# Kernel optimization log

Measured on AMD Instinct MI355X. Metric: run time of the kernel, lower is better.

## Reference

```python
import jax, jax.numpy as jnp
import numpy as np
from jax import lax


def fps_indices(points, num_sample):
    """Farthest point sampling. points: [B, C, N] -> indices [B, num_sample] int32.
    Standard PointNet++ algorithm: start at index 0, iteratively pick the point
    farthest (in squared L2) from the already-selected set."""
    B, C, N = points.shape

    def step(carry, _):
        min_d, far = carry  # min_d: [B, N] running min sq-dist, far: [B] current index
        # gather coordinates of current farthest point: [B, C, 1]
        cur = jnp.take_along_axis(points, far[:, None, None].astype(jnp.int32), axis=2)
        d = jnp.sum((points - cur) ** 2, axis=1)  # [B, N]
        min_d = jnp.minimum(min_d, d)
        nxt = jnp.argmax(min_d, axis=1).astype(jnp.int32)  # [B]
        return (min_d, nxt), far

    init = (jnp.full((B, N), 1e10, dtype=points.dtype),
            jnp.zeros((B,), dtype=jnp.int32))
    _, idx = lax.scan(step, init, None, length=num_sample)  # idx: [S, B]
    return idx.T  # [B, S]


def setup_inputs() -> dict:
    key = jax.random.key(0)
    B, C, N = 8, 3, 131072
    points = jax.random.normal(key, (B, C, N), dtype=jnp.float32)
    return {"points": points, "num_sample": 2048}


def reference(points, num_sample):
    B, C, N = points.shape
    idx = fps_indices(points, num_sample)  # [B, S]
    # gather sampled points: [B, C, S]
    gather_idx = jnp.broadcast_to(idx[:, None, :], (B, C, num_sample))
    samples = jnp.take_along_axis(points, gather_idx, axis=2)
    return samples
```

## Files before the change

kernel.cpp:

```cpp
#include <hip/hip_runtime.h>
#include <stdint.h>


#define BATCHES 8
#define NPTS    131072
#define KBLK    64
#define TPB     64
#define CHUNK   (NPTS / KBLK)
#define PPT     (CHUNK / TPB)
#define CAP     64

__global__ __launch_bounds__(TPB) void fps_kernel(
    const float* __restrict__ pts, float* __restrict__ out,
    unsigned long long* __restrict__ ws, int S)
{
    const int gb   = blockIdx.x;
    const int b    = gb & (BATCHES - 1);
    const int blk  = gb >> 3;
    const int lane = threadIdx.x;

    const float* X = pts + (size_t)(b * 3 + 0) * NPTS;
    const float* Y = pts + (size_t)(b * 3 + 1) * NPTS;
    const float* Z = pts + (size_t)(b * 3 + 2) * NPTS;
    float* outb = out + (size_t)b * 3 * S;

    const int base2 = blk * CHUNK + lane * PPT;

    float px[PPT], py[PPT], pz[PPT], md[PPT];
#pragma unroll
    for (int q = 0; q < PPT / 4; ++q) {
        float4 vx = *reinterpret_cast<const float4*>(&X[base2 + 4 * q]);
        float4 vy = *reinterpret_cast<const float4*>(&Y[base2 + 4 * q]);
        float4 vz = *reinterpret_cast<const float4*>(&Z[base2 + 4 * q]);
        px[4*q+0] = vx.x; px[4*q+1] = vx.y; px[4*q+2] = vx.z; px[4*q+3] = vx.w;
        py[4*q+0] = vy.x; py[4*q+1] = vy.y; py[4*q+2] = vy.z; py[4*q+3] = vy.w;
        pz[4*q+0] = vz.x; pz[4*q+1] = vz.y; pz[4*q+2] = vz.z; pz[4*q+3] = vz.w;
    }
#pragma unroll
    for (int k = 0; k < PPT; ++k) md[k] = 1e10f;

    unsigned long long* const agnP[2] = {
        ws + (size_t)b * KBLK,
        ws + (size_t)(BATCHES + b) * KBLK };
    volatile unsigned long long* const fstP[2] = {
        (volatile unsigned long long*)(ws + (size_t)(2 * BATCHES + b) * KBLK),
        (volatile unsigned long long*)(ws + (size_t)(3 * BATCHES + b) * KBLK) };

    float cx = X[0], cy = Y[0], cz = Z[0];
    if (blk == 0 && lane == 0) {
        outb[0]             = cx;
        outb[(size_t)S]     = cy;
        outb[(size_t)2 * S] = cz;
    }

    for (int t = 0; t < S - 1; ++t) {
        float bv = -1.0f;
        int   bk = 0;
#pragma unroll
        for (int k = 0; k < PPT; ++k) {
            float dx = __fsub_rn(px[k], cx);
            float dy = __fsub_rn(py[k], cy);
            float dz = __fsub_rn(pz[k], cz);
            float d  = __fadd_rn(__fadd_rn(__fmul_rn(dx, dx), __fmul_rn(dy, dy)),
                                 __fmul_rn(dz, dz));
            float m  = fminf(md[k], d);
            md[k] = m;
            if (m > bv) { bv = m; bk = k; }
        }
        const int bi = base2 + bk;

        float v = bv;
#pragma unroll
        for (int off = 32; off >= 1; off >>= 1)
            v = fmaxf(v, __shfl_xor(v, off));
        unsigned long long eq = __ballot(bv == v);
        int   flane = __ffsll((unsigned long long)eq) - 1;
        int   widx  = __shfl(bi, flane);

        const unsigned long long tagv = (unsigned long long)(t + 1);
        const unsigned long long mypk =
            ((unsigned long long)__float_as_uint(v) << 32) |
            ((unsigned long long)(unsigned)(0x1FFFF - widx) << 12) | tagv;

        volatile unsigned long long* fst = fstP[t & 1];
        unsigned long long*          agn = agnP[t & 1];

        if (lane == 0) fst[blk] = mypk;

        unsigned long long g;
        {
            int  spins  = 0;
            bool capped = false;
            for (;;) {
                unsigned long long gf = fst[lane];
                bool ok = ((gf & 0xFFFull) == tagv);
                if (capped && !ok) {
                    unsigned long long ga = __hip_atomic_load(&agn[lane],
                        __ATOMIC_RELAXED, __HIP_MEMORY_SCOPE_AGENT);
                    if ((ga & 0xFFFull) == tagv) { gf = ga; ok = true; }
                }
                g = gf;
                if (__all((int)ok)) break;
                if (!capped && ++spins == CAP) {
                    capped = true;
                    if (lane == 0)
                        __hip_atomic_store(&agn[blk], mypk,
                            __ATOMIC_RELAXED, __HIP_MEMORY_SCOPE_AGENT);
                }
            }
        }

        float gv = __uint_as_float((unsigned)(g >> 32));
        float m2 = gv;
#pragma unroll
        for (int off = 32; off >= 1; off >>= 1)
            m2 = fmaxf(m2, __shfl_xor(m2, off));
        unsigned long long eq2 = __ballot(gv == m2);
        int fl = __ffsll((unsigned long long)eq2) - 1;
        unsigned long long win = __shfl(g, fl);

        int far = 0x1FFFF - (int)((win >> 12) & 0x1FFFF);
        far = __builtin_amdgcn_readfirstlane(far);

        cx = X[far]; cy = Y[far]; cz = Z[far];
        if (blk == 0 && lane == 0) {
            outb[(size_t)(t + 1)]         = cx;
            outb[(size_t)S + (t + 1)]     = cy;
            outb[(size_t)2 * S + (t + 1)] = cz;
        }
    }
}

extern "C" void kernel_launch(void* const* d_in, const int* in_sizes, int n_in,
                              void* d_out, int out_size, void* d_ws, size_t ws_size,
                              hipStream_t stream) {
    const float* pts = (const float*)d_in[0];
    float* out = (float*)d_out;
    unsigned long long* ws = (unsigned long long*)d_ws;
    int S = out_size / (BATCHES * 3);

    hipMemsetAsync(d_ws, 0,
                   (size_t)4 * BATCHES * KBLK * sizeof(unsigned long long),
                   stream);

    void* args[] = { (void*)&pts, (void*)&out, (void*)&ws, (void*)&S };
    hipLaunchCooperativeKernel((const void*)fps_kernel,
                               dim3(BATCHES * KBLK), dim3(TPB),
                               args, 0, stream);
}
```

Measured before the change: 3.915 ms.

## Halve grid-wide blocks using two-wave blocks with LDS pre-reduction

After: 7.362 ms. 1.88x slower.

```diff
diff --git a/kernel.cpp b/kernel.cpp
--- a/kernel.cpp
+++ b/kernel.cpp
@@ -3,9 +3,10 @@
 
 
 #define BATCHES 8
+#define KBLK    32
+#define TPB     128
+#define NWAVE   (TPB / 64)
 #define NPTS    131072
-#define KBLK    64
-#define TPB     64
 #define CHUNK   (NPTS / KBLK)
 #define PPT     (CHUNK / TPB)
 #define CAP     64
@@ -17,14 +18,17 @@
     const int gb   = blockIdx.x;
     const int b    = gb & (BATCHES - 1);
     const int blk  = gb >> 3;
-    const int lane = threadIdx.x;
+    const int tid  = threadIdx.x;
+    const int lane = tid & 63;
+    const int wv   = tid >> 6;
+    const int myslot = lane & (KBLK - 1);
 
     const float* X = pts + (size_t)(b * 3 + 0) * NPTS;
     const float* Y = pts + (size_t)(b * 3 + 1) * NPTS;
     const float* Z = pts + (size_t)(b * 3 + 2) * NPTS;
     float* outb = out + (size_t)b * 3 * S;
 
-    const int base2 = blk * CHUNK + lane * PPT;
+    const int base2 = blk * CHUNK + tid * PPT;
 
     float px[PPT], py[PPT], pz[PPT], md[PPT];
 #pragma unroll
@@ -39,6 +43,8 @@
 #pragma unroll
     for (int k = 0; k < PPT; ++k) md[k] = 1e10f;
 
+    __shared__ unsigned long long s_part[2][NWAVE];
+
     unsigned long long* const agnP[2] = {
         ws + (size_t)b * KBLK,
         ws + (size_t)(BATCHES + b) * KBLK };
@@ -47,7 +53,7 @@
         (volatile unsigned long long*)(ws + (size_t)(3 * BATCHES + b) * KBLK) };
 
     float cx = X[0], cy = Y[0], cz = Z[0];
-    if (blk == 0 && lane == 0) {
+    if (blk == 0 && tid == 0) {
         outb[0]             = cx;
         outb[(size_t)S]     = cy;
         outb[(size_t)2 * S] = cz;
@@ -74,36 +80,50 @@
         for (int off = 32; off >= 1; off >>= 1)
             v = fmaxf(v, __shfl_xor(v, off));
         unsigned long long eq = __ballot(bv == v);
-        int   flane = __ffsll((unsigned long long)eq) - 1;
-        int   widx  = __shfl(bi, flane);
+        int flane = __ffsll(eq) - 1;
+        int widx  = __shfl(bi, flane);
+
+        const int par = t & 1;
+        if (lane == 0)
+            s_part[par][wv] =
+                ((unsigned long long)__float_as_uint(v) << 32) |
+                ((unsigned long long)(unsigned)(0x1FFFF - widx) << 12);
+        __syncthreads();
+        unsigned long long bp = s_part[par][0];
+        unsigned long long o1 = s_part[par][1];
+        if (o1 > bp) bp = o1;
 
         const unsigned long long tagv = (unsigned long long)(t + 1);
-        const unsigned long long mypk =
-            ((unsigned long long)__float_as_uint(v) << 32) |
-            ((unsigned long long)(unsigned)(0x1FFFF - widx) << 12) | tagv;
-
-        volatile unsigned long long* fst = fstP[t & 1];
-        unsigned long long*          agn = agnP[t & 1];
-
-        if (lane == 0) fst[blk] = mypk;
+        const unsigned long long mypk = bp | tagv;
+        volatile unsigned long long* fst = fstP[par];
+        unsigned long long*          agn = agnP[par];
+        if (tid == 0) fst[blk] = mypk;
 
         unsigned long long g;
         {
             int  spins  = 0;
             bool capped = false;
+            unsigned long long g0 = fst[myslot];
             for (;;) {
-                unsigned long long gf = fst[lane];
-                bool ok = ((gf & 0xFFFull) == tagv);
-                if (capped && !ok) {
-                    unsigned long long ga = __hip_atomic_load(&agn[lane],
+                unsigned long long g1 = fst[myslot];
+                if (capped && (g0 & 0xFFFull) != tagv) {
+                    unsigned long long ga = __hip_atomic_load(&agn[myslot],
                         __ATOMIC_RELAXED, __HIP_MEMORY_SCOPE_AGENT);
-                    if ((ga & 0xFFFull) == tagv) { gf = ga; ok = true; }
+                    if ((ga & 0xFFFull) == tagv) g0 = ga;
                 }
-                g = gf;
-                if (__all((int)ok)) break;
-                if (!capped && ++spins == CAP) {
+                if (__all((int)((g0 & 0xFFFull) == tagv))) { g = g0; break; }
+                unsigned long long g2 = fst[myslot];
+                if (capped && (g1 & 0xFFFull) != tagv) {
+                    unsigned long long ga = __hip_atomic_load(&agn[myslot],
+                        __ATOMIC_RELAXED, __HIP_MEMORY_SCOPE_AGENT);
+                    if ((ga & 0xFFFull) == tagv) g1 = ga;
+                }
+                if (__all((int)((g1 & 0xFFFull) == tagv))) { g = g1; break; }
+                g0 = g2;
+                spins += 2;
+                if (!capped && spins >= CAP) {
                     capped = true;
-                    if (lane == 0)
+                    if (tid == 0)
                         __hip_atomic_store(&agn[blk], mypk,
                             __ATOMIC_RELAXED, __HIP_MEMORY_SCOPE_AGENT);
                 }
@@ -116,14 +136,14 @@
         for (int off = 32; off >= 1; off >>= 1)
             m2 = fmaxf(m2, __shfl_xor(m2, off));
         unsigned long long eq2 = __ballot(gv == m2);
-        int fl = __ffsll((unsigned long long)eq2) - 1;
+        int fl = __ffsll(eq2) - 1;
         unsigned long long win = __shfl(g, fl);
 
         int far = 0x1FFFF - (int)((win >> 12) & 0x1FFFF);
         far = __builtin_amdgcn_readfirstlane(far);
 
         cx = X[far]; cy = Y[far]; cz = Z[far];
-        if (blk == 0 && lane == 0) {
+        if (blk == 0 && tid == 0) {
             outb[(size_t)(t + 1)]         = cx;
             outb[(size_t)S + (t + 1)]     = cy;
             outb[(size_t)2 * S + (t + 1)] = cz;
```

## Replace all-to-all flag polling with leader reduction and broadcast per batch

Applied to the files above, without the earlier changes.

Result: slower. 5.061 ms (+29.3%).

```diff
diff --git a/kernel.cpp b/kernel.cpp
--- a/kernel.cpp
+++ b/kernel.cpp
@@ -3,12 +3,13 @@
 
 
 #define BATCHES 8
-#define NPTS    131072
 #define KBLK    64
 #define TPB     64
+#define NPTS    131072
 #define CHUNK   (NPTS / KBLK)
 #define PPT     (CHUNK / TPB)
 #define CAP     64
+
 
 __global__ __launch_bounds__(TPB) void fps_kernel(
     const float* __restrict__ pts, float* __restrict__ out,
@@ -39,12 +40,18 @@
 #pragma unroll
     for (int k = 0; k < PPT; ++k) md[k] = 1e10f;
 
-    unsigned long long* const agnP[2] = {
+    unsigned long long* const asl[2] = {
         ws + (size_t)b * KBLK,
-        ws + (size_t)(BATCHES + b) * KBLK };
-    volatile unsigned long long* const fstP[2] = {
-        (volatile unsigned long long*)(ws + (size_t)(2 * BATCHES + b) * KBLK),
-        (volatile unsigned long long*)(ws + (size_t)(3 * BATCHES + b) * KBLK) };
+        ws + 512 + (size_t)b * KBLK };
+    volatile unsigned long long* const fsl[2] = {
+        (volatile unsigned long long*)(ws + 1024 + (size_t)b * KBLK),
+        (volatile unsigned long long*)(ws + 1536 + (size_t)b * KBLK) };
+    volatile unsigned long long* const fbc[2] = {
+        (volatile unsigned long long*)(ws + 2048 + (size_t)b * 8),
+        (volatile unsigned long long*)(ws + 2112 + (size_t)b * 8) };
+    unsigned long long* const abc[2] = {
+        ws + 2176 + (size_t)b * 8,
+        ws + 2240 + (size_t)b * 8 };
 
     float cx = X[0], cy = Y[0], cz = Z[0];
     if (blk == 0 && lane == 0) {
@@ -74,52 +81,79 @@
         for (int off = 32; off >= 1; off >>= 1)
             v = fmaxf(v, __shfl_xor(v, off));
         unsigned long long eq = __ballot(bv == v);
-        int   flane = __ffsll((unsigned long long)eq) - 1;
-        int   widx  = __shfl(bi, flane);
+        int flane = __ffsll(eq) - 1;
+        int widx  = __shfl(bi, flane);
 
+        const int par = t & 1;
         const unsigned long long tagv = (unsigned long long)(t + 1);
         const unsigned long long mypk =
             ((unsigned long long)__float_as_uint(v) << 32) |
             ((unsigned long long)(unsigned)(0x1FFFF - widx) << 12) | tagv;
 
-        volatile unsigned long long* fst = fstP[t & 1];
-        unsigned long long*          agn = agnP[t & 1];
+        if (lane == 0) fsl[par][blk] = mypk;
 
-        if (lane == 0) fst[blk] = mypk;
+        int far;
+        if (blk == 0) {
+            unsigned long long g;
+            {
+                int  spins  = 0;
+                bool capped = false;
+                for (;;) {
+                    unsigned long long gf = fsl[par][lane];
+                    bool ok = ((gf & 0xFFFull) == tagv);
+                    if (capped && !ok) {
+                        unsigned long long ga = __hip_atomic_load(&asl[par][lane],
+                            __ATOMIC_RELAXED, __HIP_MEMORY_SCOPE_AGENT);
+                        if ((ga & 0xFFFull) == tagv) { gf = ga; ok = true; }
+                    }
+                    g = gf;
+                    if (__all((int)ok)) break;
+                    if (!capped && ++spins == CAP) capped = true;
+                }
+            }
+            float gv = __uint_as_float((unsigned)(g >> 32));
+            float m2 = gv;
+#pragma unroll
+            for (int off = 32; off >= 1; off >>= 1)
+                m2 = fmaxf(m2, __shfl_xor(m2, off));
+            unsigned long long eq2 = __ballot(gv == m2);
+            int fl = __ffsll(eq2) - 1;
+            unsigned long long win = __shfl(g, fl);
+            far = 0x1FFFF - (int)((win >> 12) & 0x1FFFF);
 
-        unsigned long long g;
-        {
+            if (lane == 0) {
+                unsigned long long w =
+                    ((unsigned long long)(unsigned)far << 12) | tagv;
+                fbc[par][0] = w;
+                __hip_atomic_store(&abc[par][0], w,
+                                   __ATOMIC_RELAXED, __HIP_MEMORY_SCOPE_AGENT);
+            }
+        } else {
             int  spins  = 0;
             bool capped = false;
             for (;;) {
-                unsigned long long gf = fst[lane];
-                bool ok = ((gf & 0xFFFull) == tagv);
-                if (capped && !ok) {
-                    unsigned long long ga = __hip_atomic_load(&agn[lane],
+                unsigned long long w = fbc[par][0];
+                if ((w & 0xFFFull) == tagv) {
+                    far = (int)((w >> 12) & 0x1FFFF);
+                    break;
+                }
+                if (capped) {
+                    unsigned long long wa = __hip_atomic_load(&abc[par][0],
                         __ATOMIC_RELAXED, __HIP_MEMORY_SCOPE_AGENT);
-                    if ((ga & 0xFFFull) == tagv) { gf = ga; ok = true; }
+                    if ((wa & 0xFFFull) == tagv) {
+                        far = (int)((wa >> 12) & 0x1FFFF);
+                        break;
+                    }
                 }
-                g = gf;
-                if (__all((int)ok)) break;
                 if (!capped && ++spins == CAP) {
                     capped = true;
                     if (lane == 0)
-                        __hip_atomic_store(&agn[blk], mypk,
+                        __hip_atomic_store(&asl[par][blk], mypk,
                             __ATOMIC_RELAXED, __HIP_MEMORY_SCOPE_AGENT);
                 }
+                __builtin_amdgcn_s_sleep(1);
             }
         }
-
-        float gv = __uint_as_float((unsigned)(g >> 32));
-        float m2 = gv;
-#pragma unroll
-        for (int off = 32; off >= 1; off >>= 1)
-            m2 = fmaxf(m2, __shfl_xor(m2, off));
-        unsigned long long eq2 = __ballot(gv == m2);
-        int fl = __ffsll((unsigned long long)eq2) - 1;
-        unsigned long long win = __shfl(g, fl);
-
-        int far = 0x1FFFF - (int)((win >> 12) & 0x1FFFF);
         far = __builtin_amdgcn_readfirstlane(far);
 
         cx = X[far]; cy = Y[far]; cz = Z[far];
@@ -139,9 +173,7 @@
     unsigned long long* ws = (unsigned long long*)d_ws;
     int S = out_size / (BATCHES * 3);
 
-    hipMemsetAsync(d_ws, 0,
-                   (size_t)4 * BATCHES * KBLK * sizeof(unsigned long long),
-                   stream);
+    hipMemsetAsync(d_ws, 0, (size_t)2304 * sizeof(unsigned long long), stream);
 
     void* args[] = { (void*)&pts, (void*)&out, (void*)&ws, (void*)&S };
     hipLaunchCooperativeKernel((const void*)fps_kernel,
```
